# Kernel tuning notes

Hardware: AMD Instinct MI355X
Metric: run time of the kernel (lower is better)

Reference implementation:

```python
import jax, jax.numpy as jnp
import numpy as np

B, S, H, E, V = 16, 512, 1024, 256, 50257


def setup_inputs() -> dict:
    key = jax.random.key(0)
    ks = jax.random.split(key, 16)
    sc = 0.02
    return {
        "x": jax.random.randint(ks[0], (B, 1), 0, V),
        "dec_hs": jax.random.normal(ks[1], (1, B, H), jnp.float32),
        "enc_output": jax.random.normal(ks[2], (S, B, H), jnp.float32),
        "emb": jax.random.normal(ks[3], (V, E), jnp.float32) * sc,
        "w1_W": jax.random.normal(ks[4], (H, H), jnp.float32) * sc,
        "w1_b": jnp.zeros((H,), jnp.float32),
        "w2_W": jax.random.normal(ks[5], (H, H), jnp.float32) * sc,
        "w2_b": jnp.zeros((H,), jnp.float32),
        "va_W": jax.random.normal(ks[6], (1, H), jnp.float32) * sc,
        "va_b": jnp.zeros((1,), jnp.float32),
        "W_ih": jax.random.normal(ks[7], (3 * H, E + H), jnp.float32) * sc,
        "W_hh": jax.random.normal(ks[8], (3 * H, H), jnp.float32) * sc,
        "b_ih": jnp.zeros((3 * H,), jnp.float32),
        "b_hh": jnp.zeros((3 * H,), jnp.float32),
        "out_W": jax.random.normal(ks[9], (V, H), jnp.float32) * sc,
        "out_b": jnp.zeros((V,), jnp.float32),
    }


def reference(x, dec_hs, enc_output, emb, w1_W, w1_b, w2_W, w2_b, va_W, va_b,
              W_ih, W_hh, b_ih, b_hh, out_W, out_b):
    # --- Bahdanau attention ---
    # dec_hs: [1,B,H], enc_output: [S,B,H]
    dec_proj = dec_hs @ w1_W.T + w1_b           # [1,B,H]
    enc_proj = enc_output @ w2_W.T + w2_b       # [S,B,H]
    score = jnp.tanh(dec_proj + enc_proj) @ va_W.T + va_b  # [S,B,1]
    score = jnp.transpose(score, (1, 0, 2))     # [B,S,1]
    attn = jax.nn.softmax(score, axis=1)        # [B,S,1]
    context = jnp.sum(attn * jnp.transpose(enc_output, (1, 0, 2)), axis=1)  # [B,H]

    # --- embedding + concat (context first, as in torch.cat([ctx, emb])) ---
    e = emb[x[:, 0]]                            # [B,E]
    gru_in = jnp.concatenate([context, e], axis=-1)  # [B,H+E]

    # --- GRU single step; NOTE: original calls self.GRU(inp) without dec_hs,
    # so the initial hidden state is zeros (faithful to the source). ---
    h0 = jnp.zeros((gru_in.shape[0], w1_W.shape[0]), gru_in.dtype)  # [B,H]
    gi = gru_in @ W_ih.T + b_ih                 # [B,3H]
    gh = h0 @ W_hh.T + b_hh                     # [B,3H]
    i_r, i_z, i_n = jnp.split(gi, 3, axis=-1)
    h_r, h_z, h_n = jnp.split(gh, 3, axis=-1)
    r = jax.nn.sigmoid(i_r + h_r)
    z = jax.nn.sigmoid(i_z + h_z)
    n = jnp.tanh(i_n + r * h_n)
    h = (1.0 - z) * n + z * h0                  # [B,H]

    fc_out = h @ out_W.T + out_b                # [B,V]
    new_dec_hs = h[None]                        # [1,B,H]
    return fc_out, new_dec_hs, attn
```

## Files before the change

kernel.cpp:

```cpp
#include <hip/hip_runtime.h>
#include <hip/hip_bf16.h>

typedef unsigned short u16;
typedef __attribute__((ext_vector_type(4))) float f32x4;
typedef __attribute__((ext_vector_type(8))) __bf16 bf16x8;
typedef __attribute__((ext_vector_type(8))) unsigned short ushort8;

#define Bb 16
#define Ss 512
#define Hh 1024
#define Ee 256
#define Vv 50257
#define Mm 8192

#define WS_ENC_BF   0
#define WS_W2_BF    16777216
#define WS_DPW      18874368
#define WS_SCORE    18939904
#define WS_GRUIN    18972672
#define WS_GI       19054592
#define WS_HA_HI    19251200
#define WS_HA_LO    19283968

__device__ __forceinline__ u16 f2bf(float f) {
  unsigned u = __float_as_uint(f);
  return (u16)((u + 0x7FFFu + ((u >> 16) & 1u)) >> 16);
}

__device__ __forceinline__ void gl2lds16(const void* g, void* l) {
  __builtin_amdgcn_global_load_lds((__attribute__((address_space(1))) void*)g,
                                   (__attribute__((address_space(3))) void*)l,
                                   16, 0, 0);
}

__global__ __launch_bounds__(256) void k_cvt2(const float* __restrict__ enc, u16* __restrict__ encb,
                                              const float* __restrict__ w2, u16* __restrict__ w2b) {
  int i = blockIdx.x * 256 + threadIdx.x;
  const float* src; u16* dst; int j;
  if (i < 1048576) { src = enc; dst = encb; j = i; }
  else             { src = w2;  dst = w2b;  j = i - 1048576; }
  const float4* s4 = (const float4*)src;
  float4 a = s4[j * 2], c = s4[j * 2 + 1];
  ushort8 o;
  o[0] = f2bf(a.x); o[1] = f2bf(a.y); o[2] = f2bf(a.z); o[3] = f2bf(a.w);
  o[4] = f2bf(c.x); o[5] = f2bf(c.y); o[6] = f2bf(c.z); o[7] = f2bf(c.w);
  *(ushort8*)(dst + j * 8) = o;
}

__global__ __launch_bounds__(256) void k_prep(const float* __restrict__ dec_hs, const float* __restrict__ w1_W,
                                              const float* __restrict__ w1_b, const float* __restrict__ w2_b,
                                              const float* __restrict__ va_b, const int* __restrict__ x,
                                              const float* __restrict__ emb, float* __restrict__ dpw,
                                              float* __restrict__ score, float* __restrict__ gru_in) {
  const int n = blockIdx.x, t = threadIdx.x;
  float acc[16];
#pragma unroll
  for (int b = 0; b < 16; ++b) acc[b] = 0.f;
#pragma unroll
  for (int i = 0; i < 4; ++i) {
    int k = t + i * 256;
    float w = w1_W[n * Hh + k];
#pragma unroll
    for (int b = 0; b < 16; ++b) acc[b] = fmaf(w, dec_hs[b * Hh + k], acc[b]);
  }
#pragma unroll
  for (int m = 1; m < 64; m <<= 1)
#pragma unroll
    for (int b = 0; b < 16; ++b) acc[b] += __shfl_xor(acc[b], m, 64);
  __shared__ float red[4][16];
  int wave = t >> 6, lane = t & 63;
  if (lane == 0)
#pragma unroll
    for (int b = 0; b < 16; ++b) red[wave][b] = acc[b];
  __syncthreads();
  if (t < 16)
    dpw[t * Hh + n] = red[0][t] + red[1][t] + red[2][t] + red[3][t] + w1_b[n] + w2_b[n];
  int fid = n * 256 + t;
  if (fid < 16384) { int b = fid >> 10, k = fid & 1023; gru_in[b * 1280 + k] = 0.f; }
  int sid = fid - 16384;
  if (sid >= 0 && sid < Mm) score[sid] = va_b[0];
  int eid = fid - 24576;
  if (eid >= 0 && eid < 4096) { int b = eid >> 8, j = eid & 255; gru_in[b * 1280 + 1024 + j] = emb[x[b] * Ee + j]; }
}

__global__ __launch_bounds__(256) void k_gemm_score(const u16* __restrict__ A, const u16* __restrict__ Bm,
                                                    const float* __restrict__ dpw, const float* __restrict__ vaW,
                                                    float* __restrict__ score) {
  __shared__ __align__(16) u16 Al[4096];
  __shared__ __align__(16) u16 Bl[4096];
  const int tid = threadIdx.x;
  const int wave = tid >> 6, lane = tid & 63;
  const int quad = lane >> 4, l16 = lane & 15;
  const int m0 = blockIdx.x * 128, n0 = blockIdx.y * 128;
  const int wm = (wave & 1) * 64, wn = (wave >> 1) * 64;

  f32x4 acc[4][4];
#pragma unroll
  for (int i = 0; i < 4; ++i)
#pragma unroll
    for (int j = 0; j < 4; ++j) acc[i][j] = (f32x4){0.f, 0.f, 0.f, 0.f};

  const u16* gA = A + (m0 + (tid >> 2)) * 1024 + (tid & 3) * 8;
  const u16* gB = Bm + (n0 + (tid >> 2)) * 1024 + (tid & 3) * 8;
  u16* lA0 = &Al[(wave * 64) * 8];
  u16* lA1 = &Al[(256 + wave * 64) * 8];
  u16* lB0 = &Bl[(wave * 64) * 8];
  u16* lB1 = &Bl[(256 + wave * 64) * 8];

  for (int kt = 0; kt < 1024; kt += 32) {
    __syncthreads();
    gl2lds16(gA + kt, lA0);
    gl2lds16(gA + 64 * 1024 + kt, lA1);
    gl2lds16(gB + kt, lB0);
    gl2lds16(gB + 64 * 1024 + kt, lB1);
    __syncthreads();
    bf16x8 af[4], bfr[4];
#pragma unroll
    for (int i = 0; i < 4; ++i) {
      af[i]  = *(const bf16x8*)&Al[(wm + i * 16 + l16) * 32 + quad * 8];
      bfr[i] = *(const bf16x8*)&Bl[(wn + i * 16 + l16) * 32 + quad * 8];
    }
#pragma unroll
    for (int i = 0; i < 4; ++i)
#pragma unroll
      for (int j = 0; j < 4; ++j)
        acc[i][j] = __builtin_amdgcn_mfma_f32_16x16x32_bf16(af[i], bfr[j], acc[i][j], 0, 0, 0);
  }

  __syncthreads();
  float* dpw_t = (float*)Al;
  float* va_t  = (float*)Bl;
  for (int idx = tid; idx < 2048; idx += 256) {
    int b = idx >> 7, nn = idx & 127;
    dpw_t[idx] = dpw[b * Hh + n0 + nn];
  }
  if (tid < 128) va_t[tid] = vaW[n0 + tid];
  __syncthreads();

  float rs[4][4];
#pragma unroll
  for (int i = 0; i < 4; ++i)
#pragma unroll
    for (int r = 0; r < 4; ++r) rs[i][r] = 0.f;
#pragma unroll
  for (int i = 0; i < 4; ++i)
#pragma unroll
    for (int j = 0; j < 4; ++j) {
      int nn = wn + j * 16 + l16;
      float va = va_t[nn];
#pragma unroll
      for (int r = 0; r < 4; ++r) {
        float xv = acc[i][j][r] + dpw_t[(quad * 4 + r) * 128 + nn];
        rs[i][r] += tanhf(xv) * va;
      }
    }
#pragma unroll
  for (int i = 0; i < 4; ++i)
#pragma unroll
    for (int r = 0; r < 4; ++r) {
      float v = rs[i][r];
      v += __shfl_xor(v, 1, 64);
      v += __shfl_xor(v, 2, 64);
      v += __shfl_xor(v, 4, 64);
      v += __shfl_xor(v, 8, 64);
      if (l16 == 0) atomicAdd(&score[m0 + wm + i * 16 + quad * 4 + r], v);
    }
}

__global__ __launch_bounds__(256) void k_softmax(const float* __restrict__ score, float* __restrict__ attn) {
  const int b = blockIdx.x, t = threadIdx.x;
  __shared__ float red[256];
  float v0 = score[t * Bb + b];
  float v1 = score[(t + 256) * Bb + b];
  red[t] = fmaxf(v0, v1);
  __syncthreads();
  for (int s = 128; s > 0; s >>= 1) { if (t < s) red[t] = fmaxf(red[t], red[t + s]); __syncthreads(); }
  float mx = red[0];
  __syncthreads();
  float e0 = expf(v0 - mx), e1 = expf(v1 - mx);
  red[t] = e0 + e1;
  __syncthreads();
  for (int s = 128; s > 0; s >>= 1) { if (t < s) red[t] += red[t + s]; __syncthreads(); }
  float inv = 1.f / red[0];
  attn[b * Ss + t] = e0 * inv;
  attn[b * Ss + t + 256] = e1 * inv;
}

__global__ __launch_bounds__(256) void k_context(const float* __restrict__ attn, const float* __restrict__ enc,
                                                 float* __restrict__ gru_in) {
  const int b = blockIdx.x, sc = blockIdx.y, t = threadIdx.x;
  const int s0 = sc * 16;
  float acc[4] = {0.f, 0.f, 0.f, 0.f};
  for (int s = s0; s < s0 + 16; ++s) {
    float a = attn[b * Ss + s];
    const float* e = enc + (s * Bb + b) * Hh;
#pragma unroll
    for (int hh = 0; hh < 4; ++hh) acc[hh] = fmaf(a, e[t + hh * 256], acc[hh]);
  }
#pragma unroll
  for (int hh = 0; hh < 4; ++hh) atomicAdd(&gru_in[b * 1280 + t + hh * 256], acc[hh]);
}

__global__ __launch_bounds__(256) void k_gi(const float* __restrict__ W_ih, const float* __restrict__ gru_in,
                                            const float* __restrict__ b_ih, float* __restrict__ gi) {
  const int n = blockIdx.x, t = threadIdx.x;
  float acc[16];
#pragma unroll
  for (int b = 0; b < 16; ++b) acc[b] = 0.f;
#pragma unroll
  for (int i = 0; i < 5; ++i) {
    int k = t + i * 256;
    float w = W_ih[n * 1280 + k];
#pragma unroll
    for (int b = 0; b < 16; ++b) acc[b] = fmaf(w, gru_in[b * 1280 + k], acc[b]);
  }
#pragma unroll
  for (int m = 1; m < 64; m <<= 1)
#pragma unroll
    for (int b = 0; b < 16; ++b) acc[b] += __shfl_xor(acc[b], m, 64);
  __shared__ float red[4][16];
  int wave = t >> 6, lane = t & 63;
  if (lane == 0)
#pragma unroll
    for (int b = 0; b < 16; ++b) red[wave][b] = acc[b];
  __syncthreads();
  if (t < 16)
    gi[t * 3072 + n] = red[0][t] + red[1][t] + red[2][t] + red[3][t] + b_ih[n];
}

__global__ __launch_bounds__(256) void k_gates(const float* __restrict__ gi, const float* __restrict__ b_hh,
                                               float* __restrict__ h_out, u16* __restrict__ hA_hi,
                                               u16* __restrict__ hA_lo) {
  int idx = blockIdx.x * 256 + threadIdx.x;
  int b = idx >> 10, j = idx & 1023;
  float ir = gi[b * 3072 + j], iz = gi[b * 3072 + 1024 + j], in_ = gi[b * 3072 + 2048 + j];
  float r = 1.f / (1.f + expf(-(ir + b_hh[j])));
  float z = 1.f / (1.f + expf(-(iz + b_hh[1024 + j])));
  float n = tanhf(in_ + r * b_hh[2048 + j]);
  float hv = (1.f - z) * n;
  h_out[idx] = hv;
  u16 hi = f2bf(hv);
  float hi_f = __uint_as_float((unsigned)hi << 16);
  u16 lo = f2bf(hv - hi_f);
  int g = j >> 3, jj = j & 7;
  hA_hi[g * 128 + b * 8 + jj] = hi;
  hA_lo[g * 128 + b * 8 + jj] = lo;
}

__global__ __launch_bounds__(256) void k_fc(const float* __restrict__ out_W, const float* __restrict__ out_b,
                                            const u16* __restrict__ hA_hi, const u16* __restrict__ hA_lo,
                                            float* __restrict__ fc) {
  const int tid = threadIdx.x;
  const int wave = tid >> 6, lane = tid & 63;
  const int quad = lane >> 4, l16 = lane & 15;
  const int v = blockIdx.x * 64 + wave * 16 + l16;
  const int vr = v < Vv ? v : (Vv - 1);
  const float* wrow = out_W + (long)vr * Hh + quad * 8;
  const u16* pa_hi = hA_hi + quad * 128 + l16 * 8;
  const u16* pa_lo = hA_lo + quad * 128 + l16 * 8;

  f32x4 acc0 = (f32x4){0.f, 0.f, 0.f, 0.f};
  f32x4 acc1 = (f32x4){0.f, 0.f, 0.f, 0.f};

#pragma unroll 4
  for (int kw = 0; kw < 32; ++kw) {
    bf16x8 a_hi = *(const bf16x8*)(pa_hi + kw * 512);
    bf16x8 a_lo = *(const bf16x8*)(pa_lo + kw * 512);
    f32x4 w0 = *(const f32x4*)(wrow + kw * 32);
    f32x4 w1 = *(const f32x4*)(wrow + kw * 32 + 4);
    union { ushort8 u; bf16x8 b; } bu;
    bu.u[0] = f2bf(w0[0]); bu.u[1] = f2bf(w0[1]); bu.u[2] = f2bf(w0[2]); bu.u[3] = f2bf(w0[3]);
    bu.u[4] = f2bf(w1[0]); bu.u[5] = f2bf(w1[1]); bu.u[6] = f2bf(w1[2]); bu.u[7] = f2bf(w1[3]);
    acc0 = __builtin_amdgcn_mfma_f32_16x16x32_bf16(a_hi, bu.b, acc0, 0, 0, 0);
    acc1 = __builtin_amdgcn_mfma_f32_16x16x32_bf16(a_lo, bu.b, acc1, 0, 0, 0);
  }

  if (v < Vv) {
    float ob = out_b[v];
#pragma unroll
    for (int r = 0; r < 4; ++r)
      fc[(long)(quad * 4 + r) * Vv + v] = acc0[r] + acc1[r] + ob;
  }
}

extern "C" void kernel_launch(void* const* d_in, const int* in_sizes, int n_in,
                              void* d_out, int out_size, void* d_ws, size_t ws_size,
                              hipStream_t stream) {
  const int*   x       = (const int*)d_in[0];
  const float* dec_hs  = (const float*)d_in[1];
  const float* enc_out = (const float*)d_in[2];
  const float* emb     = (const float*)d_in[3];
  const float* w1_W    = (const float*)d_in[4];
  const float* w1_b    = (const float*)d_in[5];
  const float* w2_W    = (const float*)d_in[6];
  const float* w2_b    = (const float*)d_in[7];
  const float* va_W    = (const float*)d_in[8];
  const float* va_b    = (const float*)d_in[9];
  const float* W_ih    = (const float*)d_in[10];
  const float* b_ih    = (const float*)d_in[12];
  const float* b_hh    = (const float*)d_in[13];
  const float* out_W   = (const float*)d_in[14];
  const float* out_b   = (const float*)d_in[15];

  char* ws = (char*)d_ws;
  u16*   enc_bf = (u16*)(ws + WS_ENC_BF);
  u16*   w2_bf  = (u16*)(ws + WS_W2_BF);
  float* dpw    = (float*)(ws + WS_DPW);
  float* score  = (float*)(ws + WS_SCORE);
  float* gru_in = (float*)(ws + WS_GRUIN);
  float* gi     = (float*)(ws + WS_GI);
  u16*   hA_hi  = (u16*)(ws + WS_HA_HI);
  u16*   hA_lo  = (u16*)(ws + WS_HA_LO);

  float* fc       = (float*)d_out;
  float* h_out    = fc + (long)Bb * Vv;
  float* attn_out = h_out + Bb * Hh;

  k_cvt2<<<4608, 256, 0, stream>>>(enc_out, enc_bf, w2_W, w2_bf);
  k_prep<<<1024, 256, 0, stream>>>(dec_hs, w1_W, w1_b, w2_b, va_b, x, emb, dpw, score, gru_in);
  k_gemm_score<<<dim3(64, 8), 256, 0, stream>>>(enc_bf, w2_bf, dpw, va_W, score);
  k_softmax<<<16, 256, 0, stream>>>(score, attn_out);
  k_context<<<dim3(16, 32), 256, 0, stream>>>(attn_out, enc_out, gru_in);
  k_gi<<<3072, 256, 0, stream>>>(W_ih, gru_in, b_ih, gi);
  k_gates<<<64, 256, 0, stream>>>(gi, b_hh, h_out, hA_hi, hA_lo);
  k_fc<<<(Vv + 63) / 64, 256, 0, stream>>>(out_W, out_b, hA_hi, hA_lo, fc);
}
```

Before: 447.5 us.

## Split FC output GEMM over K into four partial blocks plus reduction kernel

The final vocabulary projection is split along the hidden dimension into four K-chunks, each computed by a separate grid row writing partial sums to workspace. A new reduction kernel adds the four partials plus bias. The aim is more blocks in flight and more memory parallelism for streaming the large fp32 out_W matrix. In exchange it adds roughly 13 MB of partial-sum writes and reads and one extra kernel launch.

New measurement: 451.0 us. About the same (+0.8%).

```diff
diff --git a/kernel.cpp b/kernel.cpp
--- a/kernel.cpp
+++ b/kernel.cpp
@@ -21,6 +21,7 @@
 #define WS_GI       19054592
 #define WS_HA_HI    19251200
 #define WS_HA_LO    19283968
+#define WS_PART     19316736
 
 __device__ __forceinline__ u16 f2bf(float f) {
   unsigned u = __float_as_uint(f);
@@ -247,23 +248,24 @@
   hA_lo[g * 128 + b * 8 + jj] = lo;
 }
 
-__global__ __launch_bounds__(256) void k_fc(const float* __restrict__ out_W, const float* __restrict__ out_b,
-                                            const u16* __restrict__ hA_hi, const u16* __restrict__ hA_lo,
-                                            float* __restrict__ fc) {
+__global__ __launch_bounds__(256) void k_fc_part(const float* __restrict__ out_W,
+                                                 const u16* __restrict__ hA_hi, const u16* __restrict__ hA_lo,
+                                                 float* __restrict__ part) {
   const int tid = threadIdx.x;
   const int wave = tid >> 6, lane = tid & 63;
   const int quad = lane >> 4, l16 = lane & 15;
   const int v = blockIdx.x * 64 + wave * 16 + l16;
+  const int kq = blockIdx.y;
   const int vr = v < Vv ? v : (Vv - 1);
-  const float* wrow = out_W + (long)vr * Hh + quad * 8;
-  const u16* pa_hi = hA_hi + quad * 128 + l16 * 8;
-  const u16* pa_lo = hA_lo + quad * 128 + l16 * 8;
+  const float* wrow = out_W + (long)vr * Hh + kq * 256 + quad * 8;
+  const u16* pa_hi = hA_hi + (kq * 32 + quad) * 128 + l16 * 8;
+  const u16* pa_lo = hA_lo + (kq * 32 + quad) * 128 + l16 * 8;
 
   f32x4 acc0 = (f32x4){0.f, 0.f, 0.f, 0.f};
   f32x4 acc1 = (f32x4){0.f, 0.f, 0.f, 0.f};
 
-#pragma unroll 4
-  for (int kw = 0; kw < 32; ++kw) {
+#pragma unroll
+  for (int kw = 0; kw < 8; ++kw) {
     bf16x8 a_hi = *(const bf16x8*)(pa_hi + kw * 512);
     bf16x8 a_lo = *(const bf16x8*)(pa_lo + kw * 512);
     f32x4 w0 = *(const f32x4*)(wrow + kw * 32);
@@ -276,10 +278,22 @@
   }
 
   if (v < Vv) {
-    float ob = out_b[v];
 #pragma unroll
     for (int r = 0; r < 4; ++r)
-      fc[(long)(quad * 4 + r) * Vv + v] = acc0[r] + acc1[r] + ob;
+      part[(long)(kq * 16 + quad * 4 + r) * Vv + v] = acc0[r] + acc1[r];
+  }
+}
+
+__global__ __launch_bounds__(256) void k_fc_red(const float* __restrict__ part, const float* __restrict__ out_b,
+                                                float* __restrict__ fc) {
+  int v = blockIdx.x * 256 + threadIdx.x;
+  int b = blockIdx.y;
+  if (v < Vv) {
+    float s = out_b[v];
+#pragma unroll
+    for (int kq = 0; kq < 4; ++kq)
+      s += part[(long)(kq * 16 + b) * Vv + v];
+    fc[(long)b * Vv + v] = s;
   }
 }
 
@@ -311,6 +325,7 @@
   float* gi     = (float*)(ws + WS_GI);
   u16*   hA_hi  = (u16*)(ws + WS_HA_HI);
   u16*   hA_lo  = (u16*)(ws + WS_HA_LO);
+  float* part   = (float*)(ws + WS_PART);
 
   float* fc       = (float*)d_out;
   float* h_out    = fc + (long)Bb * Vv;
@@ -323,5 +338,6 @@
   k_context<<<dim3(16, 32), 256, 0, stream>>>(attn_out, enc_out, gru_in);
   k_gi<<<3072, 256, 0, stream>>>(W_ih, gru_in, b_ih, gi);
   k_gates<<<64, 256, 0, stream>>>(gi, b_hh, h_out, hA_hi, hA_lo);
-  k_fc<<<(Vv + 63) / 64, 256, 0, stream>>>(out_W, out_b, hA_hi, hA_lo, fc);
-}
+  k_fc_part<<<dim3((Vv + 63) / 64, 4), 256, 0, stream>>>(out_W, hA_hi, hA_lo, part);
+  k_fc_red<<<dim3((Vv + 255) / 256, 16), 256, 0, stream>>>(part, out_b, fc);
+}
```
